# Performance work log

Measured on AMD Instinct MI355X. Metric: run time of the kernel, lower is better.

Reference implementation:

```python
import jax, jax.numpy as jnp
import numpy as np

N_NODES = 100000


def sage_conv(x, src, dst, w_self, w_neigh, b):
    # DGL SAGEConv with 'mean' aggregator: out = x @ W_self + mean_neigh(x) @ W_neigh + b
    msg = x[src]                                                     # [E, d] gather
    agg = jax.ops.segment_sum(msg, dst, num_segments=N_NODES)        # [N, d]
    deg = jax.ops.segment_sum(jnp.ones((src.shape[0],), x.dtype), dst,
                              num_segments=N_NODES)                  # [N]
    h_neigh = agg / jnp.maximum(deg, 1.0)[:, None]                   # mean; 0 for isolated nodes
    return x @ w_self + h_neigh @ w_neigh + b


def setup_inputs() -> dict:
    key = jax.random.key(0)
    ks = jax.random.split(key, 12)
    N, E = N_NODES, 1600000
    in_f, h_f, r_f = 128, 128, 64
    glorot = lambda k, i, o: jax.random.normal(k, (i, o), jnp.float32) / np.float32(np.sqrt(i))
    return {
        "in_feat": jax.random.normal(ks[0], (N, in_f), jnp.float32),
        "src": jax.random.randint(ks[1], (E,), 0, N),
        "dst": jax.random.randint(ks[2], (E,), 0, N),
        "w1_self": glorot(ks[3], in_f, h_f), "w1_neigh": glorot(ks[4], in_f, h_f), "b1": jnp.zeros((h_f,), jnp.float32),
        "w2_self": glorot(ks[5], h_f, r_f), "w2_neigh": glorot(ks[6], h_f, r_f), "b2": jnp.zeros((r_f,), jnp.float32),
        "w3_self": glorot(ks[7], r_f, r_f), "w3_neigh": glorot(ks[8], r_f, r_f), "b3": jnp.zeros((r_f,), jnp.float32),
    }


def reference(in_feat, src, dst,
              w1_self, w1_neigh, b1,
              w2_self, w2_neigh, b2,
              w3_self, w3_neigh, b3):
    h = sage_conv(in_feat, src, dst, w1_self, w1_neigh, b1)
    h = jax.nn.relu(h)
    h = sage_conv(h, src, dst, w2_self, w2_neigh, b2)
    h = jax.nn.relu(h)
    # dropout is treated as identity (deterministic eval-mode reference)
    h = sage_conv(h, src, dst, w3_self, w3_neigh, b3)
    return jax.nn.softmax(h, axis=-1)
```

## Files before the change

### kernel.cpp

```cpp
#include <hip/hip_runtime.h>
#include <hip/hip_bf16.h>

#define N_NODES 100000

typedef unsigned short ushort_t;
typedef __attribute__((ext_vector_type(8))) short short8;
typedef __attribute__((ext_vector_type(4))) float f32x4;

static __device__ __forceinline__ ushort_t f2bf(float f) {
    unsigned u = __float_as_uint(f);
    unsigned r = u + 0x7FFFu + ((u >> 16) & 1u);
    return (ushort_t)(r >> 16);
}
static __device__ __forceinline__ float bf2f(ushort_t h) {
    return __uint_as_float(((unsigned)h) << 16);
}

static __device__ __forceinline__ void split8(const float* __restrict__ xp,
                                              short8& hi, short8& lo) {
    float4 x0 = *(const float4*)xp;
    float4 x1 = *(const float4*)(xp + 4);
    float xs[8] = {x0.x, x0.y, x0.z, x0.w, x1.x, x1.y, x1.z, x1.w};
    #pragma unroll
    for (int j = 0; j < 8; ++j) {
        ushort_t h = f2bf(xs[j]);
        hi[j] = (short)h;
        lo[j] = (short)f2bf(xs[j] - bf2f(h));
    }
}

static __device__ __forceinline__ void acc_u32(unsigned w, float& a0, float& a1) {
    a0 += __uint_as_float(w << 16);
    a1 += __uint_as_float(w & 0xFFFF0000u);
}


__global__ __launch_bounds__(256) void scan_partial_sums(const int* __restrict__ deg,
                                                         int* __restrict__ partials, int N) {
    __shared__ int wsums[4];
    int tid = threadIdx.x, lane = tid & 63, wv = tid >> 6;
    int i0 = blockIdx.x * 1024 + tid * 4;
    int s = 0;
    #pragma unroll
    for (int j = 0; j < 4; ++j) {
        int i = i0 + j;
        if (i < N) s += deg[i];
    }
    #pragma unroll
    for (int off = 32; off > 0; off >>= 1) s += __shfl_xor(s, off, 64);
    if (lane == 0) wsums[wv] = s;
    __syncthreads();
    if (tid == 0)
        partials[blockIdx.x] = wsums[0] + wsums[1] + wsums[2] + wsums[3];
}

__global__ __launch_bounds__(256) void scan_partials(int* __restrict__ partials, int NB,
                                                     int* __restrict__ row_ptr, int N) {
    __shared__ int wsums[4];
    int tid = threadIdx.x, lane = tid & 63, wv = tid >> 6;
    int v = (tid < NB) ? partials[tid] : 0;
    int x = v;
    #pragma unroll
    for (int off = 1; off < 64; off <<= 1) {
        int y = __shfl_up(x, off, 64);
        if (lane >= off) x += y;
    }
    if (lane == 63) wsums[wv] = x;
    __syncthreads();
    int woff = 0;
    for (int w = 0; w < wv; ++w) woff += wsums[w];
    int incl = x + woff;
    if (tid < NB) partials[tid] = incl - v;
    if (tid == NB - 1) row_ptr[N] = incl;
}

__global__ __launch_bounds__(256) void scan_emit(const int* __restrict__ deg,
                                                 const int* __restrict__ partials,
                                                 int* __restrict__ row_ptr,
                                                 int* __restrict__ cursor,
                                                 float* __restrict__ inv_deg,
                                                 int* __restrict__ gcur, int N) {
    __shared__ int wsums[4];
    int tid = threadIdx.x, lane = tid & 63, wv = tid >> 6;
    int i0 = blockIdx.x * 1024 + tid * 4;
    int d[4];
    #pragma unroll
    for (int j = 0; j < 4; ++j) {
        int i = i0 + j;
        d[j] = (i < N) ? deg[i] : 0;
    }
    int s = d[0] + d[1] + d[2] + d[3];
    int x = s;
    #pragma unroll
    for (int off = 1; off < 64; off <<= 1) {
        int y = __shfl_up(x, off, 64);
        if (lane >= off) x += y;
    }
    if (lane == 63) wsums[wv] = x;
    __syncthreads();
    int woff = 0;
    for (int w = 0; w < wv; ++w) woff += wsums[w];
    int run = partials[blockIdx.x] + woff + x - s;
    #pragma unroll
    for (int j = 0; j < 4; ++j) {
        int i = i0 + j;
        if (i < N) {
            row_ptr[i] = run;
            cursor[i]  = run;
            inv_deg[i] = 1.0f / (float)(d[j] > 0 ? d[j] : 1);
            if ((i & 255) == 0) gcur[i >> 8] = run;
            run += d[j];
        }
    }
}

#define MAXBUCK 512
__global__ __launch_bounds__(256) void bin_pairs(const int* __restrict__ src,
                                                 const int* __restrict__ dst,
                                                 int* __restrict__ gcur,
                                                 long long* __restrict__ staged,
                                                 int E, int NBUCK, int C) {
    __shared__ int cnt[MAXBUCK];
    int tid = threadIdx.x;
    int e0 = blockIdx.x * C;
    int e1 = min(e0 + C, E);
    for (int b = tid; b < NBUCK; b += 256) cnt[b] = 0;
    __syncthreads();
    for (int e = e0 + tid; e < e1; e += 256) {
        int d = __builtin_nontemporal_load(&dst[e]);
        atomicAdd(&cnt[d >> 8], 1);
    }
    __syncthreads();
    for (int b = tid; b < NBUCK; b += 256) {
        int c = cnt[b];
        cnt[b] = (c > 0) ? atomicAdd(&gcur[b], c) : 0;
    }
    __syncthreads();
    for (int e = e0 + tid; e < e1; e += 256) {
        int d = __builtin_nontemporal_load(&dst[e]);
        int s = __builtin_nontemporal_load(&src[e]);
        int p = atomicAdd(&cnt[d >> 8], 1);
        staged[p] = ((long long)d << 32) | (unsigned)s;
    }
}

__global__ __launch_bounds__(256) void scatter_bucket(const long long* __restrict__ staged,
                                                      const int* __restrict__ row_ptr,
                                                      int* __restrict__ cursor,
                                                      int* __restrict__ edge_src,
                                                      int N) {
    int b = blockIdx.x;
    int lo = b << 8;
    int hiN = min((b + 1) << 8, N);
    int gstart = row_ptr[lo];
    int gend   = row_ptr[hiN];
    for (int p = gstart + threadIdx.x; p < gend; p += 256) {
        long long pr = __builtin_nontemporal_load(&staged[p]);
        int d = (int)(pr >> 32);
        int s = (int)(pr & 0xFFFFFFFFll);
        int pos = atomicAdd(&cursor[d], 1);
        edge_src[pos] = s;
    }
}

__global__ __launch_bounds__(256) void pack_hist(
        const float* __restrict__ W0, const float* __restrict__ W1,
        const float* __restrict__ W2, const float* __restrict__ W3,
        const float* __restrict__ W4, const float* __restrict__ W5,
        ushort_t* H0, ushort_t* L0, ushort_t* H1, ushort_t* L1,
        ushort_t* H2, ushort_t* L2, ushort_t* H3, ushort_t* L3,
        ushort_t* H4, ushort_t* L4, ushort_t* H5, ushort_t* L5,
        const int* __restrict__ dst, int* __restrict__ deg, int E) {
    int b = blockIdx.x;
    if (b >= 28) {
        int e = (b - 28) * 256 + threadIdx.x;
        if (e < E) atomicAdd(&deg[__builtin_nontemporal_load(&dst[e])], 1);
        return;
    }
    const float* W; ushort_t* Hi; ushort_t* Lo; int K, NS, base;
    if (b < 8)       { W = W0; Hi = H0; Lo = L0; K = 128; NS = 128; base = 0;  }
    else if (b < 16) { W = W1; Hi = H1; Lo = L1; K = 128; NS = 128; base = 8;  }
    else if (b < 20) { W = W2; Hi = H2; Lo = L2; K = 128; NS = 64;  base = 16; }
    else if (b < 24) { W = W3; Hi = H3; Lo = L3; K = 128; NS = 64;  base = 20; }
    else if (b < 26) { W = W4; Hi = H4; Lo = L4; K = 64;  NS = 64;  base = 24; }
    else             { W = W5; Hi = H5; Lo = L5; K = 64;  NS = 64;  base = 26; }
    int tid = (b - base) * 256 + threadIdx.x;
    if (tid >= (K * NS) / 8) return;
    int l  = tid & 63;
    int fl = tid >> 6;
    int NT = NS / 16;
    int t = fl % NT, s = fl / NT;
    ushort_t hs[8], ls[8];
    #pragma unroll
    for (int j = 0; j < 8; ++j) {
        int k = s * 32 + (l >> 4) * 8 + j;
        int n = t * 16 + (l & 15);
        float w = W[(size_t)k * NS + n];
        ushort_t h = f2bf(w);
        hs[j] = h;
        ls[j] = f2bf(w - bf2f(h));
    }
    #pragma unroll
    for (int j = 0; j < 8; ++j) {
        Hi[(size_t)tid * 8 + j] = hs[j];
        Lo[(size_t)tid * 8 + j] = ls[j];
    }
}

template <int K, int NS>
__global__ __launch_bounds__(256) void mfma_gemm(const float* __restrict__ X,
                                                 const ushort_t* __restrict__ BsHi,
                                                 const ushort_t* __restrict__ BsLo,
                                                 const ushort_t* __restrict__ BnHi,
                                                 const ushort_t* __restrict__ BnLo,
                                                 const float* __restrict__ bias,
                                                 float* __restrict__ S,
                                                 ushort_t* __restrict__ Zb,
                                                 int M) {
    constexpr int KS = K / 32;
    constexpr int NT = NS / 16;
    __shared__ float ldsS[4][32 * 20];
    __shared__ float ldsZ[4][32 * 20];
    int tid = threadIdx.x;
    int lane = tid & 63, w = tid >> 6;
    int baseM = blockIdx.x * 128 + w * 32;
    int rIn = lane & 15, q = lane >> 4;
    float* bufS = ldsS[w];
    float* bufZ = ldsZ[w];

    short8 Ahi[KS][2], Alo[KS][2];
    #pragma unroll
    for (int s = 0; s < KS; ++s) {
        #pragma unroll
        for (int mt = 0; mt < 2; ++mt) {
            int gm = baseM + mt * 16 + rIn;
            if (gm < M) {
                split8(&X[(size_t)gm * K + s * 32 + q * 8], Ahi[s][mt], Alo[s][mt]);
            } else {
                #pragma unroll
                for (int j = 0; j < 8; ++j) { Ahi[s][mt][j] = 0; Alo[s][mt][j] = 0; }
            }
        }
    }

    for (int t = 0; t < NT; ++t) {
        f32x4 aS0 = {0.f, 0.f, 0.f, 0.f}, aS1 = {0.f, 0.f, 0.f, 0.f};
        f32x4 aZ0 = {0.f, 0.f, 0.f, 0.f}, aZ1 = {0.f, 0.f, 0.f, 0.f};
        #pragma unroll
        for (int s = 0; s < KS; ++s) {
            size_t fo = ((size_t)(s * NT + t) * 64 + lane) * 8;
            short8 bsh = *(const short8*)&BsHi[fo];
            short8 bsl = *(const short8*)&BsLo[fo];
            short8 bnh = *(const short8*)&BnHi[fo];
            short8 bnl = *(const short8*)&BnLo[fo];
            aS0 = __builtin_amdgcn_mfma_f32_16x16x32_bf16(Ahi[s][0], bsh, aS0, 0, 0, 0);
            aS0 = __builtin_amdgcn_mfma_f32_16x16x32_bf16(Alo[s][0], bsh, aS0, 0, 0, 0);
            aS0 = __builtin_amdgcn_mfma_f32_16x16x32_bf16(Ahi[s][0], bsl, aS0, 0, 0, 0);
            aS1 = __builtin_amdgcn_mfma_f32_16x16x32_bf16(Ahi[s][1], bsh, aS1, 0, 0, 0);
            aS1 = __builtin_amdgcn_mfma_f32_16x16x32_bf16(Alo[s][1], bsh, aS1, 0, 0, 0);
            aS1 = __builtin_amdgcn_mfma_f32_16x16x32_bf16(Ahi[s][1], bsl, aS1, 0, 0, 0);
            aZ0 = __builtin_amdgcn_mfma_f32_16x16x32_bf16(Ahi[s][0], bnh, aZ0, 0, 0, 0);
            aZ0 = __builtin_amdgcn_mfma_f32_16x16x32_bf16(Alo[s][0], bnh, aZ0, 0, 0, 0);
            aZ0 = __builtin_amdgcn_mfma_f32_16x16x32_bf16(Ahi[s][0], bnl, aZ0, 0, 0, 0);
            aZ1 = __builtin_amdgcn_mfma_f32_16x16x32_bf16(Ahi[s][1], bnh, aZ1, 0, 0, 0);
            aZ1 = __builtin_amdgcn_mfma_f32_16x16x32_bf16(Alo[s][1], bnh, aZ1, 0, 0, 0);
            aZ1 = __builtin_amdgcn_mfma_f32_16x16x32_bf16(Ahi[s][1], bnl, aZ1, 0, 0, 0);
        }
        #pragma unroll
        for (int r = 0; r < 4; ++r) {
            bufS[(q * 4 + r) * 20 + rIn]        = aS0[r];
            bufS[(16 + q * 4 + r) * 20 + rIn]   = aS1[r];
            bufZ[(q * 4 + r) * 20 + rIn]        = aZ0[r];
            bufZ[(16 + q * 4 + r) * 20 + rIn]   = aZ1[r];
        }
        int row = lane >> 2;
        int cq  = lane & 3;
        int col = t * 16 + cq * 4;
        float4 bv = *(const float4*)&bias[col];
        #pragma unroll
        for (int half = 0; half < 2; ++half) {
            int gm = baseM + half * 16 + row;
            float4 v = *(float4*)&bufS[(half * 16 + row) * 20 + cq * 4];
            float4 z = *(float4*)&bufZ[(half * 16 + row) * 20 + cq * 4];
            if (gm < M) {
                float4 o;
                o.x = v.x + bv.x; o.y = v.y + bv.y;
                o.z = v.z + bv.z; o.w = v.w + bv.w;
                *(float4*)&S[(size_t)gm * NS + col] = o;
                uint2 o2;
                o2.x = (unsigned)f2bf(z.x) | ((unsigned)f2bf(z.y) << 16);
                o2.y = (unsigned)f2bf(z.z) | ((unsigned)f2bf(z.w) << 16);
                *(uint2*)&Zb[(size_t)gm * NS + col] = o2;
            }
        }
    }
}

template <int D, int ACT>
__global__ __launch_bounds__(256) void agg_kernel(const float* __restrict__ S,
                                                  const ushort_t* __restrict__ Zb,
                                                  const int* __restrict__ row_ptr,
                                                  const int* __restrict__ edge_src,
                                                  const float* __restrict__ inv_deg,
                                                  float* __restrict__ out, int N) {
    constexpr int G  = D / 8;
    constexpr int PF = 8;
    constexpr int NG = 256 / G;
    constexpr int U  = G;
    int tid = threadIdx.x;
    int g = tid / G, fl = tid % G;
    int n = blockIdx.x * NG + g;
    if (n >= N) return;
    int beg = row_ptr[n], end = row_ptr[n + 1];
    float id = inv_deg[n];

    const f32x4* Sp = (const f32x4*)(S + (size_t)n * D) + fl * 2;
    f32x4 s40 = __builtin_nontemporal_load(Sp);
    f32x4 s41 = __builtin_nontemporal_load(Sp + 1);

    float acc[2][PF];
    #pragma unroll
    for (int i = 0; i < PF; ++i) { acc[0][i] = 0.f; acc[1][i] = 0.f; }

    const char* zlane = (const char*)Zb + fl * 16;

    for (int j = beg; j < end; j += U) {
        int je = j + fl;
        int myS = (je < end) ? __builtin_nontemporal_load(&edge_src[je]) : -1;
        uint4 u[U];
        #pragma unroll
        for (int k = 0; k < U; ++k) {
            int s = __shfl(myS, k, U);
            u[k] = make_uint4(0u, 0u, 0u, 0u);
            if (s >= 0)
                u[k] = *(const uint4*)(zlane + ((size_t)((unsigned)s) * (D * 2)));
        }
        #pragma unroll
        for (int k = 0; k < U; ++k) {
            acc_u32(u[k].x, acc[k & 1][0], acc[k & 1][1]);
            acc_u32(u[k].y, acc[k & 1][2], acc[k & 1][3]);
            acc_u32(u[k].z, acc[k & 1][4], acc[k & 1][5]);
            acc_u32(u[k].w, acc[k & 1][6], acc[k & 1][7]);
        }
    }

    float v[PF];
    #pragma unroll
    for (int i = 0; i < 4; ++i) {
        v[i]     = s40[i] + id * (acc[0][i]     + acc[1][i]);
        v[4 + i] = s41[i] + id * (acc[0][4 + i] + acc[1][4 + i]);
    }

    float4* Op = (float4*)(out + (size_t)n * D) + fl * 2;
    if constexpr (ACT == 0) {
        float4 o0, o1;
        o0.x = fmaxf(v[0], 0.f); o0.y = fmaxf(v[1], 0.f);
        o0.z = fmaxf(v[2], 0.f); o0.w = fmaxf(v[3], 0.f);
        o1.x = fmaxf(v[4], 0.f); o1.y = fmaxf(v[5], 0.f);
        o1.z = fmaxf(v[6], 0.f); o1.w = fmaxf(v[7], 0.f);
        Op[0] = o0; Op[1] = o1;
    } else {
        float m = v[0];
        #pragma unroll
        for (int i = 1; i < 8; ++i) m = fmaxf(m, v[i]);
        #pragma unroll
        for (int off = 4; off > 0; off >>= 1) m = fmaxf(m, __shfl_xor(m, off, 8));
        float e[8], s = 0.f;
        #pragma unroll
        for (int i = 0; i < 8; ++i) { e[i] = __expf(v[i] - m); s += e[i]; }
        #pragma unroll
        for (int off = 4; off > 0; off >>= 1) s += __shfl_xor(s, off, 8);
        float inv = 1.0f / s;
        float4 o0, o1;
        o0.x = e[0] * inv; o0.y = e[1] * inv; o0.z = e[2] * inv; o0.w = e[3] * inv;
        o1.x = e[4] * inv; o1.y = e[5] * inv; o1.z = e[6] * inv; o1.w = e[7] * inv;
        Op[0] = o0; Op[1] = o1;
    }
}

extern "C" void kernel_launch(void* const* d_in, const int* in_sizes, int n_in,
                              void* d_out, int out_size, void* d_ws, size_t ws_size,
                              hipStream_t stream) {
    const float* in_feat = (const float*)d_in[0];
    const int*   src     = (const int*)d_in[1];
    const int*   dst     = (const int*)d_in[2];
    const float* w1s = (const float*)d_in[3];
    const float* w1n = (const float*)d_in[4];
    const float* b1  = (const float*)d_in[5];
    const float* w2s = (const float*)d_in[6];
    const float* w2n = (const float*)d_in[7];
    const float* b2  = (const float*)d_in[8];
    const float* w3s = (const float*)d_in[9];
    const float* w3n = (const float*)d_in[10];
    const float* b3  = (const float*)d_in[11];

    const int N = N_NODES;
    const int E = in_sizes[1];

    char* p = (char*)d_ws;
    auto carve = [&](size_t bytes) -> char* {
        char* q = p;
        p += (bytes + 511) & ~(size_t)511;
        return q;
    };
    float*    S        = (float*)   carve((size_t)N * 128 * sizeof(float));
    ushort_t* Zb       = (ushort_t*)carve((size_t)N * 128 * sizeof(ushort_t));
    float*    H        = (float*)   carve((size_t)N * 128 * sizeof(float));
    int*      edge_src = (int*)     carve((size_t)E * sizeof(int));
    int*      row_ptr  = (int*)     carve((size_t)(N + 1) * sizeof(int));
    int*      cursor   = (int*)     carve((size_t)N * sizeof(int));
    int*      deg      = (int*)     carve((size_t)N * sizeof(int));
    float*    invd     = (float*)   carve((size_t)N * sizeof(float));
    int*      partials = (int*)     carve(256 * sizeof(int));
    int*      gcur     = (int*)     carve(MAXBUCK * sizeof(int));
    long long* staged  = (long long*)H;
    ushort_t* P1sH = (ushort_t*)carve(128 * 128 * 2); ushort_t* P1sL = (ushort_t*)carve(128 * 128 * 2);
    ushort_t* P1nH = (ushort_t*)carve(128 * 128 * 2); ushort_t* P1nL = (ushort_t*)carve(128 * 128 * 2);
    ushort_t* P2sH = (ushort_t*)carve(128 * 64 * 2);  ushort_t* P2sL = (ushort_t*)carve(128 * 64 * 2);
    ushort_t* P2nH = (ushort_t*)carve(128 * 64 * 2);  ushort_t* P2nL = (ushort_t*)carve(128 * 64 * 2);
    ushort_t* P3sH = (ushort_t*)carve(64 * 64 * 2);   ushort_t* P3sL = (ushort_t*)carve(64 * 64 * 2);
    ushort_t* P3nH = (ushort_t*)carve(64 * 64 * 2);   ushort_t* P3nL = (ushort_t*)carve(64 * 64 * 2);

    (void)hipMemsetAsync(deg, 0, (size_t)N * sizeof(int), stream);
    pack_hist<<<28 + (E + 255) / 256, 256, 0, stream>>>(
        w1s, w1n, w2s, w2n, w3s, w3n,
        P1sH, P1sL, P1nH, P1nL,
        P2sH, P2sL, P2nH, P2nL,
        P3sH, P3sL, P3nH, P3nL,
        dst, deg, E);
    const int NB = (N + 1023) / 1024;
    scan_partial_sums<<<NB, 256, 0, stream>>>(deg, partials, N);
    scan_partials<<<1, 256, 0, stream>>>(partials, NB, row_ptr, N);
    scan_emit<<<NB, 256, 0, stream>>>(deg, partials, row_ptr, cursor, invd, gcur, N);
    const int NBUCK = (N + 255) >> 8;
    const int BINB  = 256;
    const int CHUNK = (E + BINB - 1) / BINB;
    bin_pairs<<<BINB, 256, 0, stream>>>(src, dst, gcur, staged, E, NBUCK, CHUNK);
    scatter_bucket<<<NBUCK, 256, 0, stream>>>(staged, row_ptr, cursor, edge_src, N);

    const int GB   = (N + 127) / 128;
    const int AB128 = (N + 15) / 16;
    const int AB64  = (N + 31) / 32;

    mfma_gemm<128, 128><<<GB, 256, 0, stream>>>(in_feat, P1sH, P1sL, P1nH, P1nL, b1, S, Zb, N);
    agg_kernel<128, 0><<<AB128, 256, 0, stream>>>(S, Zb, row_ptr, edge_src, invd, H, N);

    mfma_gemm<128, 64><<<GB, 256, 0, stream>>>(H, P2sH, P2sL, P2nH, P2nL, b2, S, Zb, N);
    agg_kernel<64, 0><<<AB64, 256, 0, stream>>>(S, Zb, row_ptr, edge_src, invd, H, N);

    mfma_gemm<64, 64><<<GB, 256, 0, stream>>>(H, P3sH, P3sL, P3nH, P3nL, b3, S, Zb, N);
    agg_kernel<64, 1><<<AB64, 256, 0, stream>>>(S, Zb, row_ptr, edge_src, invd,
                                                (float*)d_out, N);
}
```

Measured before the change: 465.8 us.

## Fuse all three SAGE layers into one cooperative persistent kernel with grid syncs

Replaces the six separate GEMM and aggregation launches with a single cooperative kernel. Each 512-node block keeps its self-term S tile in LDS and writes only the bf16 neighbour projection Z to global memory, with grid.sync between phases. Layer 1 is split into two 64-column halves so everything fits in the 64-wide buffers. This removes the S round-trip through HBM and the launch gaps, at the cost of grid-wide barriers, a large LDS footprint, and 196 blocks of 512 threads that must all be co-resident. Layer 1's gather pass now runs twice, once per column half.

```diff
diff --git a/kernel.cpp b/kernel.cpp
--- a/kernel.cpp
+++ b/kernel.cpp
@@ -1,7 +1,12 @@
 #include <hip/hip_runtime.h>
 #include <hip/hip_bf16.h>
+#include <hip/hip_cooperative_groups.h>
+
+namespace cg = cooperative_groups;
 
 #define N_NODES 100000
+#define NPB 512
+#define FGRID ((N_NODES + NPB - 1) / NPB)
 
 typedef unsigned short ushort_t;
 typedef __attribute__((ext_vector_type(8))) short short8;
@@ -207,175 +212,203 @@
     }
 }
 
-template <int K, int NS>
-__global__ __launch_bounds__(256) void mfma_gemm(const float* __restrict__ X,
-                                                 const ushort_t* __restrict__ BsHi,
-                                                 const ushort_t* __restrict__ BsLo,
-                                                 const ushort_t* __restrict__ BnHi,
-                                                 const ushort_t* __restrict__ BnLo,
-                                                 const float* __restrict__ bias,
-                                                 float* __restrict__ S,
-                                                 ushort_t* __restrict__ Zb,
-                                                 int M) {
+template <int K, int NTW>
+static __device__ __forceinline__ void gemm_phase(
+        const float* __restrict__ X,
+        const ushort_t* __restrict__ BsHi, const ushort_t* __restrict__ BsLo,
+        const ushort_t* __restrict__ BnHi, const ushort_t* __restrict__ BnLo,
+        const float* __restrict__ bias, int colBase, int tileBase,
+        float* __restrict__ Sl, ushort_t* __restrict__ Zg,
+        float* __restrict__ bufZ, int nodeBase, int N, int tid) {
     constexpr int KS = K / 32;
-    constexpr int NT = NS / 16;
-    __shared__ float ldsS[4][32 * 20];
-    __shared__ float ldsZ[4][32 * 20];
-    int tid = threadIdx.x;
     int lane = tid & 63, w = tid >> 6;
-    int baseM = blockIdx.x * 128 + w * 32;
     int rIn = lane & 15, q = lane >> 4;
-    float* bufS = ldsS[w];
-    float* bufZ = ldsZ[w];
-
-    short8 Ahi[KS][2], Alo[KS][2];
-    #pragma unroll
-    for (int s = 0; s < KS; ++s) {
-        #pragma unroll
-        for (int mt = 0; mt < 2; ++mt) {
-            int gm = baseM + mt * 16 + rIn;
-            if (gm < M) {
-                split8(&X[(size_t)gm * K + s * 32 + q * 8], Ahi[s][mt], Alo[s][mt]);
-            } else {
-                #pragma unroll
-                for (int j = 0; j < 8; ++j) { Ahi[s][mt][j] = 0; Alo[s][mt][j] = 0; }
-            }
-        }
-    }
-
-    for (int t = 0; t < NT; ++t) {
-        f32x4 aS0 = {0.f, 0.f, 0.f, 0.f}, aS1 = {0.f, 0.f, 0.f, 0.f};
-        f32x4 aZ0 = {0.f, 0.f, 0.f, 0.f}, aZ1 = {0.f, 0.f, 0.f, 0.f};
+    float* bufZw = bufZ + w * 640;
+    #pragma unroll
+    for (int p = 0; p < 2; ++p) {
+        int rowBase = p * 256 + w * 32;
+        int gmBase = nodeBase + rowBase;
+        short8 Ahi[KS][2], Alo[KS][2];
         #pragma unroll
         for (int s = 0; s < KS; ++s) {
-            size_t fo = ((size_t)(s * NT + t) * 64 + lane) * 8;
-            short8 bsh = *(const short8*)&BsHi[fo];
-            short8 bsl = *(const short8*)&BsLo[fo];
-            short8 bnh = *(const short8*)&BnHi[fo];
-            short8 bnl = *(const short8*)&BnLo[fo];
-            aS0 = __builtin_amdgcn_mfma_f32_16x16x32_bf16(Ahi[s][0], bsh, aS0, 0, 0, 0);
-            aS0 = __builtin_amdgcn_mfma_f32_16x16x32_bf16(Alo[s][0], bsh, aS0, 0, 0, 0);
-            aS0 = __builtin_amdgcn_mfma_f32_16x16x32_bf16(Ahi[s][0], bsl, aS0, 0, 0, 0);
-            aS1 = __builtin_amdgcn_mfma_f32_16x16x32_bf16(Ahi[s][1], bsh, aS1, 0, 0, 0);
-            aS1 = __builtin_amdgcn_mfma_f32_16x16x32_bf16(Alo[s][1], bsh, aS1, 0, 0, 0);
-            aS1 = __builtin_amdgcn_mfma_f32_16x16x32_bf16(Ahi[s][1], bsl, aS1, 0, 0, 0);
-            aZ0 = __builtin_amdgcn_mfma_f32_16x16x32_bf16(Ahi[s][0], bnh, aZ0, 0, 0, 0);
-            aZ0 = __builtin_amdgcn_mfma_f32_16x16x32_bf16(Alo[s][0], bnh, aZ0, 0, 0, 0);
-            aZ0 = __builtin_amdgcn_mfma_f32_16x16x32_bf16(Ahi[s][0], bnl, aZ0, 0, 0, 0);
-            aZ1 = __builtin_amdgcn_mfma_f32_16x16x32_bf16(Ahi[s][1], bnh, aZ1, 0, 0, 0);
-            aZ1 = __builtin_amdgcn_mfma_f32_16x16x32_bf16(Alo[s][1], bnh, aZ1, 0, 0, 0);
-            aZ1 = __builtin_amdgcn_mfma_f32_16x16x32_bf16(Ahi[s][1], bnl, aZ1, 0, 0, 0);
+            #pragma unroll
+            for (int mt = 0; mt < 2; ++mt) {
+                int gm = gmBase + mt * 16 + rIn;
+                if (gm < N) {
+                    split8(&X[(size_t)gm * K + s * 32 + q * 8], Ahi[s][mt], Alo[s][mt]);
+                } else {
+                    #pragma unroll
+                    for (int j = 0; j < 8; ++j) { Ahi[s][mt][j] = 0; Alo[s][mt][j] = 0; }
+                }
+            }
         }
         #pragma unroll
-        for (int r = 0; r < 4; ++r) {
-            bufS[(q * 4 + r) * 20 + rIn]        = aS0[r];
-            bufS[(16 + q * 4 + r) * 20 + rIn]   = aS1[r];
-            bufZ[(q * 4 + r) * 20 + rIn]        = aZ0[r];
-            bufZ[(16 + q * 4 + r) * 20 + rIn]   = aZ1[r];
+        for (int t = 0; t < 4; ++t) {
+            f32x4 aS0 = {0.f, 0.f, 0.f, 0.f}, aS1 = {0.f, 0.f, 0.f, 0.f};
+            f32x4 aZ0 = {0.f, 0.f, 0.f, 0.f}, aZ1 = {0.f, 0.f, 0.f, 0.f};
+            #pragma unroll
+            for (int s = 0; s < KS; ++s) {
+                size_t fo = ((size_t)(s * NTW + tileBase + t) * 64 + lane) * 8;
+                short8 bsh = *(const short8*)&BsHi[fo];
+                short8 bsl = *(const short8*)&BsLo[fo];
+                short8 bnh = *(const short8*)&BnHi[fo];
+                short8 bnl = *(const short8*)&BnLo[fo];
+                aS0 = __builtin_amdgcn_mfma_f32_16x16x32_bf16(Ahi[s][0], bsh, aS0, 0, 0, 0);
+                aS0 = __builtin_amdgcn_mfma_f32_16x16x32_bf16(Alo[s][0], bsh, aS0, 0, 0, 0);
+                aS0 = __builtin_amdgcn_mfma_f32_16x16x32_bf16(Ahi[s][0], bsl, aS0, 0, 0, 0);
+                aS1 = __builtin_amdgcn_mfma_f32_16x16x32_bf16(Ahi[s][1], bsh, aS1, 0, 0, 0);
+                aS1 = __builtin_amdgcn_mfma_f32_16x16x32_bf16(Alo[s][1], bsh, aS1, 0, 0, 0);
+                aS1 = __builtin_amdgcn_mfma_f32_16x16x32_bf16(Ahi[s][1], bsl, aS1, 0, 0, 0);
+                aZ0 = __builtin_amdgcn_mfma_f32_16x16x32_bf16(Ahi[s][0], bnh, aZ0, 0, 0, 0);
+                aZ0 = __builtin_amdgcn_mfma_f32_16x16x32_bf16(Alo[s][0], bnh, aZ0, 0, 0, 0);
+                aZ0 = __builtin_amdgcn_mfma_f32_16x16x32_bf16(Ahi[s][0], bnl, aZ0, 0, 0, 0);
+                aZ1 = __builtin_amdgcn_mfma_f32_16x16x32_bf16(Ahi[s][1], bnh, aZ1, 0, 0, 0);
+                aZ1 = __builtin_amdgcn_mfma_f32_16x16x32_bf16(Alo[s][1], bnh, aZ1, 0, 0, 0);
+                aZ1 = __builtin_amdgcn_mfma_f32_16x16x32_bf16(Ahi[s][1], bnl, aZ1, 0, 0, 0);
+            }
+            float bv = bias[colBase + t * 16 + rIn];
+            #pragma unroll
+            for (int r = 0; r < 4; ++r) {
+                Sl[(rowBase + q * 4 + r) * 64 + t * 16 + rIn]      = aS0[r] + bv;
+                Sl[(rowBase + 16 + q * 4 + r) * 64 + t * 16 + rIn] = aS1[r] + bv;
+                bufZw[(q * 4 + r) * 20 + rIn]      = aZ0[r];
+                bufZw[(16 + q * 4 + r) * 20 + rIn] = aZ1[r];
+            }
+            int row = lane >> 2, cq = lane & 3;
+            int col = t * 16 + cq * 4;
+            #pragma unroll
+            for (int half = 0; half < 2; ++half) {
+                int gm = gmBase + half * 16 + row;
+                float4 z = *(float4*)&bufZw[(half * 16 + row) * 20 + cq * 4];
+                if (gm < N) {
+                    uint2 o2;
+                    o2.x = (unsigned)f2bf(z.x) | ((unsigned)f2bf(z.y) << 16);
+                    o2.y = (unsigned)f2bf(z.z) | ((unsigned)f2bf(z.w) << 16);
+                    *(uint2*)&Zg[(size_t)gm * 64 + col] = o2;
+                }
+            }
         }
-        int row = lane >> 2;
-        int cq  = lane & 3;
-        int col = t * 16 + cq * 4;
-        float4 bv = *(const float4*)&bias[col];
+    }
+}
+
+template <int ACT>
+static __device__ __forceinline__ void agg_phase(
+        const float* __restrict__ Sl,
+        const ushort_t* __restrict__ Zg,
+        const int* __restrict__ row_ptr, const int* __restrict__ edge_src,
+        const float* __restrict__ invd,
+        float* __restrict__ outp, int outStride, int outColBase,
+        int nodeBase, int N, int tid) {
+    int g = tid >> 3, fl = tid & 7;
+    const char* zlane = (const char*)Zg + fl * 16;
+    #pragma unroll 1
+    for (int pass = 0; pass < 8; ++pass) {
+        int nl = pass * 64 + g;
+        int n = nodeBase + nl;
+        bool act = (n < N);
+        int beg = 0, end = 0;
+        float id = 0.f;
+        if (act) { beg = row_ptr[n]; end = row_ptr[n + 1]; id = invd[n]; }
+        float acc[2][8];
         #pragma unroll
-        for (int half = 0; half < 2; ++half) {
-            int gm = baseM + half * 16 + row;
-            float4 v = *(float4*)&bufS[(half * 16 + row) * 20 + cq * 4];
-            float4 z = *(float4*)&bufZ[(half * 16 + row) * 20 + cq * 4];
-            if (gm < M) {
-                float4 o;
-                o.x = v.x + bv.x; o.y = v.y + bv.y;
-                o.z = v.z + bv.z; o.w = v.w + bv.w;
-                *(float4*)&S[(size_t)gm * NS + col] = o;
-                uint2 o2;
-                o2.x = (unsigned)f2bf(z.x) | ((unsigned)f2bf(z.y) << 16);
-                o2.y = (unsigned)f2bf(z.z) | ((unsigned)f2bf(z.w) << 16);
-                *(uint2*)&Zb[(size_t)gm * NS + col] = o2;
+        for (int i = 0; i < 8; ++i) { acc[0][i] = 0.f; acc[1][i] = 0.f; }
+        for (int j = beg; j < end; j += 8) {
+            int je = j + fl;
+            int myS = (je < end) ? __builtin_nontemporal_load(&edge_src[je]) : -1;
+            uint4 u[8];
+            #pragma unroll
+            for (int k = 0; k < 8; ++k) {
+                int s = __shfl(myS, k, 8);
+                u[k] = make_uint4(0u, 0u, 0u, 0u);
+                if (s >= 0)
+                    u[k] = *(const uint4*)(zlane + ((size_t)((unsigned)s) << 7));
+            }
+            #pragma unroll
+            for (int k = 0; k < 8; ++k) {
+                acc_u32(u[k].x, acc[k & 1][0], acc[k & 1][1]);
+                acc_u32(u[k].y, acc[k & 1][2], acc[k & 1][3]);
+                acc_u32(u[k].z, acc[k & 1][4], acc[k & 1][5]);
+                acc_u32(u[k].w, acc[k & 1][6], acc[k & 1][7]);
             }
         }
-    }
-}
-
-template <int D, int ACT>
-__global__ __launch_bounds__(256) void agg_kernel(const float* __restrict__ S,
-                                                  const ushort_t* __restrict__ Zb,
-                                                  const int* __restrict__ row_ptr,
-                                                  const int* __restrict__ edge_src,
-                                                  const float* __restrict__ inv_deg,
-                                                  float* __restrict__ out, int N) {
-    constexpr int G  = D / 8;
-    constexpr int PF = 8;
-    constexpr int NG = 256 / G;
-    constexpr int U  = G;
+        if (act) {
+            const f32x4* Sp = (const f32x4*)(Sl + nl * 64 + fl * 8);
+            f32x4 s40 = Sp[0], s41 = Sp[1];
+            float v[8];
+            #pragma unroll
+            for (int i = 0; i < 4; ++i) {
+                v[i]     = s40[i] + id * (acc[0][i]     + acc[1][i]);
+                v[4 + i] = s41[i] + id * (acc[0][4 + i] + acc[1][4 + i]);
+            }
+            float4* Op = (float4*)(outp + (size_t)n * outStride + outColBase) + fl * 2;
+            if constexpr (ACT == 0) {
+                float4 o0, o1;
+                o0.x = fmaxf(v[0], 0.f); o0.y = fmaxf(v[1], 0.f);
+                o0.z = fmaxf(v[2], 0.f); o0.w = fmaxf(v[3], 0.f);
+                o1.x = fmaxf(v[4], 0.f); o1.y = fmaxf(v[5], 0.f);
+                o1.z = fmaxf(v[6], 0.f); o1.w = fmaxf(v[7], 0.f);
+                Op[0] = o0; Op[1] = o1;
+            } else {
+                float m = v[0];
+                #pragma unroll
+                for (int i = 1; i < 8; ++i) m = fmaxf(m, v[i]);
+                #pragma unroll
+                for (int off = 4; off > 0; off >>= 1) m = fmaxf(m, __shfl_xor(m, off, 8));
+                float e[8], s = 0.f;
+                #pragma unroll
+                for (int i = 0; i < 8; ++i) { e[i] = __expf(v[i] - m); s += e[i]; }
+                #pragma unroll
+                for (int off = 4; off > 0; off >>= 1) s += __shfl_xor(s, off, 8);
+                float inv = 1.0f / s;
+                float4 o0, o1;
+                o0.x = e[0] * inv; o0.y = e[1] * inv; o0.z = e[2] * inv; o0.w = e[3] * inv;
+                o1.x = e[4] * inv; o1.y = e[5] * inv; o1.z = e[6] * inv; o1.w = e[7] * inv;
+                Op[0] = o0; Op[1] = o1;
+            }
+        }
+    }
+}
+
+__global__ __launch_bounds__(512, 2) void fused3(
+        const float* __restrict__ X,
+        const ushort_t* __restrict__ P1sH, const ushort_t* __restrict__ P1sL,
+        const ushort_t* __restrict__ P1nH, const ushort_t* __restrict__ P1nL,
+        const float* __restrict__ b1,
+        const ushort_t* __restrict__ P2sH, const ushort_t* __restrict__ P2sL,
+        const ushort_t* __restrict__ P2nH, const ushort_t* __restrict__ P2nL,
+        const float* __restrict__ b2,
+        const ushort_t* __restrict__ P3sH, const ushort_t* __restrict__ P3sL,
+        const ushort_t* __restrict__ P3nH, const ushort_t* __restrict__ P3nL,
+        const float* __restrict__ b3,
+        const int* __restrict__ row_ptr, const int* __restrict__ edge_src,
+        const float* __restrict__ invd,
+        ushort_t* __restrict__ Z0, ushort_t* __restrict__ Z1,
+        float* __restrict__ H1, float* __restrict__ H2,
+        float* __restrict__ out, int N) {
+    __shared__ float Sl[NPB * 64];
+    __shared__ float bufZ[8 * 640];
+    cg::grid_group grid = cg::this_grid();
     int tid = threadIdx.x;
-    int g = tid / G, fl = tid % G;
-    int n = blockIdx.x * NG + g;
-    if (n >= N) return;
-    int beg = row_ptr[n], end = row_ptr[n + 1];
-    float id = inv_deg[n];
-
-    const f32x4* Sp = (const f32x4*)(S + (size_t)n * D) + fl * 2;
-    f32x4 s40 = __builtin_nontemporal_load(Sp);
-    f32x4 s41 = __builtin_nontemporal_load(Sp + 1);
-
-    float acc[2][PF];
-    #pragma unroll
-    for (int i = 0; i < PF; ++i) { acc[0][i] = 0.f; acc[1][i] = 0.f; }
-
-    const char* zlane = (const char*)Zb + fl * 16;
-
-    for (int j = beg; j < end; j += U) {
-        int je = j + fl;
-        int myS = (je < end) ? __builtin_nontemporal_load(&edge_src[je]) : -1;
-        uint4 u[U];
-        #pragma unroll
-        for (int k = 0; k < U; ++k) {
-            int s = __shfl(myS, k, U);
-            u[k] = make_uint4(0u, 0u, 0u, 0u);
-            if (s >= 0)
-                u[k] = *(const uint4*)(zlane + ((size_t)((unsigned)s) * (D * 2)));
-        }
-        #pragma unroll
-        for (int k = 0; k < U; ++k) {
-            acc_u32(u[k].x, acc[k & 1][0], acc[k & 1][1]);
-            acc_u32(u[k].y, acc[k & 1][2], acc[k & 1][3]);
-            acc_u32(u[k].z, acc[k & 1][4], acc[k & 1][5]);
-            acc_u32(u[k].w, acc[k & 1][6], acc[k & 1][7]);
-        }
-    }
-
-    float v[PF];
-    #pragma unroll
-    for (int i = 0; i < 4; ++i) {
-        v[i]     = s40[i] + id * (acc[0][i]     + acc[1][i]);
-        v[4 + i] = s41[i] + id * (acc[0][4 + i] + acc[1][4 + i]);
-    }
-
-    float4* Op = (float4*)(out + (size_t)n * D) + fl * 2;
-    if constexpr (ACT == 0) {
-        float4 o0, o1;
-        o0.x = fmaxf(v[0], 0.f); o0.y = fmaxf(v[1], 0.f);
-        o0.z = fmaxf(v[2], 0.f); o0.w = fmaxf(v[3], 0.f);
-        o1.x = fmaxf(v[4], 0.f); o1.y = fmaxf(v[5], 0.f);
-        o1.z = fmaxf(v[6], 0.f); o1.w = fmaxf(v[7], 0.f);
-        Op[0] = o0; Op[1] = o1;
-    } else {
-        float m = v[0];
-        #pragma unroll
-        for (int i = 1; i < 8; ++i) m = fmaxf(m, v[i]);
-        #pragma unroll
-        for (int off = 4; off > 0; off >>= 1) m = fmaxf(m, __shfl_xor(m, off, 8));
-        float e[8], s = 0.f;
-        #pragma unroll
-        for (int i = 0; i < 8; ++i) { e[i] = __expf(v[i] - m); s += e[i]; }
-        #pragma unroll
-        for (int off = 4; off > 0; off >>= 1) s += __shfl_xor(s, off, 8);
-        float inv = 1.0f / s;
-        float4 o0, o1;
-        o0.x = e[0] * inv; o0.y = e[1] * inv; o0.z = e[2] * inv; o0.w = e[3] * inv;
-        o1.x = e[4] * inv; o1.y = e[5] * inv; o1.z = e[6] * inv; o1.w = e[7] * inv;
-        Op[0] = o0; Op[1] = o1;
-    }
+    int nodeBase = blockIdx.x * NPB;
+
+    gemm_phase<128, 8>(X, P1sH, P1sL, P1nH, P1nL, b1, 0, 0, Sl, Z0, bufZ, nodeBase, N, tid);
+    grid.sync();
+    agg_phase<0>(Sl, Z0, row_ptr, edge_src, invd, H1, 128, 0, nodeBase, N, tid);
+    __syncthreads();
+
+    gemm_phase<128, 8>(X, P1sH, P1sL, P1nH, P1nL, b1, 64, 4, Sl, Z1, bufZ, nodeBase, N, tid);
+    grid.sync();
+    agg_phase<0>(Sl, Z1, row_ptr, edge_src, invd, H1, 128, 64, nodeBase, N, tid);
+    grid.sync();
+
+    gemm_phase<128, 4>(H1, P2sH, P2sL, P2nH, P2nL, b2, 0, 0, Sl, Z0, bufZ, nodeBase, N, tid);
+    grid.sync();
+    agg_phase<0>(Sl, Z0, row_ptr, edge_src, invd, H2, 64, 0, nodeBase, N, tid);
+    grid.sync();
+
+    gemm_phase<64, 4>(H2, P3sH, P3sL, P3nH, P3nL, b3, 0, 0, Sl, Z1, bufZ, nodeBase, N, tid);
+    grid.sync();
+    agg_phase<1>(Sl, Z1, row_ptr, edge_src, invd, out, 64, 0, nodeBase, N, tid);
 }
 
 extern "C" void kernel_launch(void* const* d_in, const int* in_sizes, int n_in,
@@ -403,9 +436,10 @@
         p += (bytes + 511) & ~(size_t)511;
         return q;
     };
-    float*    S        = (float*)   carve((size_t)N * 128 * sizeof(float));
-    ushort_t* Zb       = (ushort_t*)carve((size_t)N * 128 * sizeof(ushort_t));
-    float*    H        = (float*)   carve((size_t)N * 128 * sizeof(float));
+    float*    H1       = (float*)   carve((size_t)N * 128 * sizeof(float));
+    float*    H2       = (float*)   carve((size_t)N * 64 * sizeof(float));
+    ushort_t* Z0       = (ushort_t*)carve((size_t)N * 64 * sizeof(ushort_t));
+    ushort_t* Z1       = (ushort_t*)carve((size_t)N * 64 * sizeof(ushort_t));
     int*      edge_src = (int*)     carve((size_t)E * sizeof(int));
     int*      row_ptr  = (int*)     carve((size_t)(N + 1) * sizeof(int));
     int*      cursor   = (int*)     carve((size_t)N * sizeof(int));
@@ -413,7 +447,7 @@
     float*    invd     = (float*)   carve((size_t)N * sizeof(float));
     int*      partials = (int*)     carve(256 * sizeof(int));
     int*      gcur     = (int*)     carve(MAXBUCK * sizeof(int));
-    long long* staged  = (long long*)H;
+    long long* staged  = (long long*)H1;
     ushort_t* P1sH = (ushort_t*)carve(128 * 128 * 2); ushort_t* P1sL = (ushort_t*)carve(128 * 128 * 2);
     ushort_t* P1nH = (ushort_t*)carve(128 * 128 * 2); ushort_t* P1nL = (ushort_t*)carve(128 * 128 * 2);
     ushort_t* P2sH = (ushort_t*)carve(128 * 64 * 2);  ushort_t* P2sL = (ushort_t*)carve(128 * 64 * 2);
@@ -438,17 +472,17 @@
     bin_pairs<<<BINB, 256, 0, stream>>>(src, dst, gcur, staged, E, NBUCK, CHUNK);
     scatter_bucket<<<NBUCK, 256, 0, stream>>>(staged, row_ptr, cursor, edge_src, N);
 
-    const int GB   = (N + 127) / 128;
-    const int AB128 = (N + 15) / 16;
-    const int AB64  = (N + 31) / 32;
-
-    mfma_gemm<128, 128><<<GB, 256, 0, stream>>>(in_feat, P1sH, P1sL, P1nH, P1nL, b1, S, Zb, N);
-    agg_kernel<128, 0><<<AB128, 256, 0, stream>>>(S, Zb, row_ptr, edge_src, invd, H, N);
-
-    mfma_gemm<128, 64><<<GB, 256, 0, stream>>>(H, P2sH, P2sL, P2nH, P2nL, b2, S, Zb, N);
-    agg_kernel<64, 0><<<AB64, 256, 0, stream>>>(S, Zb, row_ptr, edge_src, invd, H, N);
-
-    mfma_gemm<64, 64><<<GB, 256, 0, stream>>>(H, P3sH, P3sL, P3nH, P3nL, b3, S, Zb, N);
-    agg_kernel<64, 1><<<AB64, 256, 0, stream>>>(S, Zb, row_ptr, edge_src, invd,
-                                                (float*)d_out, N);
-}
+    int Nv = N;
+    float* outp = (float*)d_out;
+    void* kargs[] = {
+        (void*)&in_feat,
+        (void*)&P1sH, (void*)&P1sL, (void*)&P1nH, (void*)&P1nL, (void*)&b1,
+        (void*)&P2sH, (void*)&P2sL, (void*)&P2nH, (void*)&P2nL, (void*)&b2,
+        (void*)&P3sH, (void*)&P3sL, (void*)&P3nH, (void*)&P3nL, (void*)&b3,
+        (void*)&row_ptr, (void*)&edge_src, (void*)&invd,
+        (void*)&Z0, (void*)&Z1, (void*)&H1, (void*)&H2,
+        (void*)&outp, (void*)&Nv
+    };
+    (void)hipLaunchCooperativeKernel((void*)fused3, dim3(FGRID), dim3(512),
+                                     kargs, 0, stream);
+}
```

Result: slower. 700.4 us (+50.4%).

## Overlap layer-1 GEMM with CSR binning and scatter kernels

Applied to the files above, without the earlier changes.

The first-layer GEMM does not depend on the CSR build, so its blocks are split in half and packed into the same launches as the edge binning and the bucket scatter kernels. Extra block indices run the GEMM body while the lower indices do the binning or scattering, and the separate GEMM launch is removed. This aims to fill idle compute units during the latency-bound atomic and scatter phases and to drop one launch. In exchange, every block of the fused kernels reserves the GEMM's shared memory and registers, which may lower occupancy for the binning and scatter work.

```diff
diff --git a/kernel.cpp b/kernel.cpp
--- a/kernel.cpp
+++ b/kernel.cpp
@@ -111,55 +111,6 @@
             if ((i & 255) == 0) gcur[i >> 8] = run;
             run += d[j];
         }
-    }
-}
-
-#define MAXBUCK 512
-__global__ __launch_bounds__(256) void bin_pairs(const int* __restrict__ src,
-                                                 const int* __restrict__ dst,
-                                                 int* __restrict__ gcur,
-                                                 long long* __restrict__ staged,
-                                                 int E, int NBUCK, int C) {
-    __shared__ int cnt[MAXBUCK];
-    int tid = threadIdx.x;
-    int e0 = blockIdx.x * C;
-    int e1 = min(e0 + C, E);
-    for (int b = tid; b < NBUCK; b += 256) cnt[b] = 0;
-    __syncthreads();
-    for (int e = e0 + tid; e < e1; e += 256) {
-        int d = __builtin_nontemporal_load(&dst[e]);
-        atomicAdd(&cnt[d >> 8], 1);
-    }
-    __syncthreads();
-    for (int b = tid; b < NBUCK; b += 256) {
-        int c = cnt[b];
-        cnt[b] = (c > 0) ? atomicAdd(&gcur[b], c) : 0;
-    }
-    __syncthreads();
-    for (int e = e0 + tid; e < e1; e += 256) {
-        int d = __builtin_nontemporal_load(&dst[e]);
-        int s = __builtin_nontemporal_load(&src[e]);
-        int p = atomicAdd(&cnt[d >> 8], 1);
-        staged[p] = ((long long)d << 32) | (unsigned)s;
-    }
-}
-
-__global__ __launch_bounds__(256) void scatter_bucket(const long long* __restrict__ staged,
-                                                      const int* __restrict__ row_ptr,
-                                                      int* __restrict__ cursor,
-                                                      int* __restrict__ edge_src,
-                                                      int N) {
-    int b = blockIdx.x;
-    int lo = b << 8;
-    int hiN = min((b + 1) << 8, N);
-    int gstart = row_ptr[lo];
-    int gend   = row_ptr[hiN];
-    for (int p = gstart + threadIdx.x; p < gend; p += 256) {
-        long long pr = __builtin_nontemporal_load(&staged[p]);
-        int d = (int)(pr >> 32);
-        int s = (int)(pr & 0xFFFFFFFFll);
-        int pos = atomicAdd(&cursor[d], 1);
-        edge_src[pos] = s;
     }
 }
 
@@ -208,25 +159,22 @@
 }
 
 template <int K, int NS>
-__global__ __launch_bounds__(256) void mfma_gemm(const float* __restrict__ X,
-                                                 const ushort_t* __restrict__ BsHi,
-                                                 const ushort_t* __restrict__ BsLo,
-                                                 const ushort_t* __restrict__ BnHi,
-                                                 const ushort_t* __restrict__ BnLo,
-                                                 const float* __restrict__ bias,
-                                                 float* __restrict__ S,
-                                                 ushort_t* __restrict__ Zb,
-                                                 int M) {
+static __device__ __forceinline__ void gemm_body(
+        int gblk,
+        const float* __restrict__ X,
+        const ushort_t* __restrict__ BsHi, const ushort_t* __restrict__ BsLo,
+        const ushort_t* __restrict__ BnHi, const ushort_t* __restrict__ BnLo,
+        const float* __restrict__ bias,
+        float* __restrict__ S, ushort_t* __restrict__ Zb, int M,
+        float* __restrict__ ldsS, float* __restrict__ ldsZ) {
     constexpr int KS = K / 32;
     constexpr int NT = NS / 16;
-    __shared__ float ldsS[4][32 * 20];
-    __shared__ float ldsZ[4][32 * 20];
     int tid = threadIdx.x;
     int lane = tid & 63, w = tid >> 6;
-    int baseM = blockIdx.x * 128 + w * 32;
+    int baseM = gblk * 128 + w * 32;
     int rIn = lane & 15, q = lane >> 4;
-    float* bufS = ldsS[w];
-    float* bufZ = ldsZ[w];
+    float* bufS = ldsS + w * 640;
+    float* bufZ = ldsZ + w * 640;
 
     short8 Ahi[KS][2], Alo[KS][2];
     #pragma unroll
@@ -293,6 +241,93 @@
                 *(uint2*)&Zb[(size_t)gm * NS + col] = o2;
             }
         }
+    }
+}
+
+template <int K, int NS>
+__global__ __launch_bounds__(256) void mfma_gemm(const float* __restrict__ X,
+                                                 const ushort_t* __restrict__ BsHi,
+                                                 const ushort_t* __restrict__ BsLo,
+                                                 const ushort_t* __restrict__ BnHi,
+                                                 const ushort_t* __restrict__ BnLo,
+                                                 const float* __restrict__ bias,
+                                                 float* __restrict__ S,
+                                                 ushort_t* __restrict__ Zb,
+                                                 int M) {
+    __shared__ float ldsS[4 * 640];
+    __shared__ float ldsZ[4 * 640];
+    gemm_body<K, NS>(blockIdx.x, X, BsHi, BsLo, BnHi, BnLo, bias, S, Zb, M, ldsS, ldsZ);
+}
+
+#define MAXBUCK 512
+__global__ __launch_bounds__(256) void bin_gemm1(
+        const int* __restrict__ src, const int* __restrict__ dst,
+        int* __restrict__ gcur, long long* __restrict__ staged,
+        int E, int NBUCK, int C,
+        const float* __restrict__ X,
+        const ushort_t* __restrict__ BsHi, const ushort_t* __restrict__ BsLo,
+        const ushort_t* __restrict__ BnHi, const ushort_t* __restrict__ BnLo,
+        const float* __restrict__ bias,
+        float* __restrict__ S, ushort_t* __restrict__ Zb, int M) {
+    __shared__ float ldsS[4 * 640];
+    __shared__ float ldsZ[4 * 640];
+    __shared__ int cnt[MAXBUCK];
+    int b = blockIdx.x;
+    if (b >= 256) {
+        gemm_body<128, 128>(b - 256, X, BsHi, BsLo, BnHi, BnLo, bias, S, Zb, M, ldsS, ldsZ);
+        return;
+    }
+    int tid = threadIdx.x;
+    int e0 = b * C;
+    int e1 = min(e0 + C, E);
+    for (int k = tid; k < NBUCK; k += 256) cnt[k] = 0;
+    __syncthreads();
+    for (int e = e0 + tid; e < e1; e += 256) {
+        int d = __builtin_nontemporal_load(&dst[e]);
+        atomicAdd(&cnt[d >> 8], 1);
+    }
+    __syncthreads();
+    for (int k = tid; k < NBUCK; k += 256) {
+        int c = cnt[k];
+        cnt[k] = (c > 0) ? atomicAdd(&gcur[k], c) : 0;
+    }
+    __syncthreads();
+    for (int e = e0 + tid; e < e1; e += 256) {
+        int d = __builtin_nontemporal_load(&dst[e]);
+        int s = __builtin_nontemporal_load(&src[e]);
+        int p = atomicAdd(&cnt[d >> 8], 1);
+        staged[p] = ((long long)d << 32) | (unsigned)s;
+    }
+}
+
+__global__ __launch_bounds__(256) void scatter_gemm1(
+        const long long* __restrict__ staged,
+        const int* __restrict__ row_ptr,
+        int* __restrict__ cursor, int* __restrict__ edge_src, int N,
+        int NBUCK, int GH,
+        const float* __restrict__ X,
+        const ushort_t* __restrict__ BsHi, const ushort_t* __restrict__ BsLo,
+        const ushort_t* __restrict__ BnHi, const ushort_t* __restrict__ BnLo,
+        const float* __restrict__ bias,
+        float* __restrict__ S, ushort_t* __restrict__ Zb, int M) {
+    __shared__ float ldsS[4 * 640];
+    __shared__ float ldsZ[4 * 640];
+    int b = blockIdx.x;
+    if (b >= NBUCK) {
+        gemm_body<128, 128>(GH + (b - NBUCK), X, BsHi, BsLo, BnHi, BnLo, bias, S, Zb, M,
+                            ldsS, ldsZ);
+        return;
+    }
+    int lo = b << 8;
+    int hiN = min((b + 1) << 8, N);
+    int gstart = row_ptr[lo];
+    int gend   = row_ptr[hiN];
+    for (int p = gstart + threadIdx.x; p < gend; p += 256) {
+        long long pr = __builtin_nontemporal_load(&staged[p]);
+        int d = (int)(pr >> 32);
+        int s = (int)(pr & 0xFFFFFFFFll);
+        int pos = atomicAdd(&cursor[d], 1);
+        edge_src[pos] = s;
     }
 }
 
@@ -432,17 +467,24 @@
     scan_partial_sums<<<NB, 256, 0, stream>>>(deg, partials, N);
     scan_partials<<<1, 256, 0, stream>>>(partials, NB, row_ptr, N);
     scan_emit<<<NB, 256, 0, stream>>>(deg, partials, row_ptr, cursor, invd, gcur, N);
+
+    const int GB    = (N + 127) / 128;
+    const int GH    = GB / 2;
     const int NBUCK = (N + 255) >> 8;
     const int BINB  = 256;
     const int CHUNK = (E + BINB - 1) / BINB;
-    bin_pairs<<<BINB, 256, 0, stream>>>(src, dst, gcur, staged, E, NBUCK, CHUNK);
-    scatter_bucket<<<NBUCK, 256, 0, stream>>>(staged, row_ptr, cursor, edge_src, N);
-
-    const int GB   = (N + 127) / 128;
+
+    bin_gemm1<<<256 + GH, 256, 0, stream>>>(
+        src, dst, gcur, staged, E, NBUCK, CHUNK,
+        in_feat, P1sH, P1sL, P1nH, P1nL, b1, S, Zb, N);
+
+    scatter_gemm1<<<NBUCK + (GB - GH), 256, 0, stream>>>(
+        staged, row_ptr, cursor, edge_src, N, NBUCK, GH,
+        in_feat, P1sH, P1sL, P1nH, P1nL, b1, S, Zb, N);
+
     const int AB128 = (N + 15) / 16;
     const int AB64  = (N + 31) / 32;
 
-    mfma_gemm<128, 128><<<GB, 256, 0, stream>>>(in_feat, P1sH, P1sL, P1nH, P1nL, b1, S, Zb, N);
     agg_kernel<128, 0><<<AB128, 256, 0, stream>>>(S, Zb, row_ptr, edge_src, invd, H, N);
 
     mfma_gemm<128, 64><<<GB, 256, 0, stream>>>(H, P2sH, P2sL, P2nH, P2nL, b2, S, Zb, N);
```

New measurement: 478.2 us. 1.03x slower.
